# Performance work log

Hardware: AMD Instinct MI355X
Metric: run time of the kernel (lower is better)

Reference implementation:

```python
import jax, jax.numpy as jnp
import numpy as np

C, H, OUT = 64, 128, 64          # in_channels, hidden_dim, out_channels
N, E = 20000, 640000             # nodes, edges
LN_EPS = 1e-5


def layer_norm(x, g, b):
    mu = jnp.mean(x, axis=-1, keepdims=True)
    var = jnp.var(x, axis=-1, keepdims=True)
    return (x - mu) * jax.lax.rsqrt(var + LN_EPS) * g + b


def setup_inputs() -> dict:
    key = jax.random.key(0)
    ks = jax.random.split(key, 12)
    F = 2 * C + 5  # edge MLP input dim = 133

    def w(k, shape, fan_in):
        return jax.random.normal(k, shape, jnp.float32) / np.float32(np.sqrt(fan_in))

    return {
        "x": jax.random.normal(ks[0], (N, C), jnp.float32),
        "pos": jax.random.normal(ks[1], (N, 2), jnp.float32),
        "vel": jax.random.normal(ks[2], (N, 2), jnp.float32),
        # phi_e: Linear(F,H) -> LN -> Softplus -> Linear(H,H) -> Softplus -> Linear(H,H)
        "We1": w(ks[3], (F, H), F), "be1": jnp.zeros((H,), jnp.float32),
        "ge1": jnp.ones((H,), jnp.float32), "bte1": jnp.zeros((H,), jnp.float32),
        "We2": w(ks[4], (H, H), H), "be2": jnp.zeros((H,), jnp.float32),
        "We3": w(ks[5], (H, H), H), "be3": jnp.zeros((H,), jnp.float32),
        # phi_v: Linear(F,H) -> LN -> Softplus -> Linear(H,1)
        "Wv1": w(ks[6], (F, H), F), "bv1": jnp.zeros((H,), jnp.float32),
        "gv1": jnp.ones((H,), jnp.float32), "btv1": jnp.zeros((H,), jnp.float32),
        "Wv2": w(ks[7], (H, 1), H), "bv2": jnp.zeros((1,), jnp.float32),
        # phi_h: Linear(C+H+1,H) -> LN -> Softplus -> Linear(H,OUT)
        "Wh1": w(ks[8], (C + H + 1, H), C + H + 1), "bh1": jnp.zeros((H,), jnp.float32),
        "gh1": jnp.ones((H,), jnp.float32), "bth1": jnp.zeros((H,), jnp.float32),
        "Wh2": w(ks[9], (H, OUT), H), "bh2": jnp.zeros((OUT,), jnp.float32),
        "edge_index": jax.random.randint(ks[10], (2, E), 0, N, dtype=jnp.int64)
        if jax.config.jax_enable_x64 else jax.random.randint(ks[10], (2, E), 0, N, dtype=jnp.int32),
    }


def reference(x, pos, vel,
              We1, be1, ge1, bte1, We2, be2, We3, be3,
              Wv1, bv1, gv1, btv1, Wv2, bv2,
              Wh1, bh1, gh1, bth1, Wh2, bh2,
              edge_index):
    src = edge_index[0]  # j (source / x_j)
    dst = edge_index[1]  # i (target / x_i, aggregation index)

    # per-edge geometric features (gather)
    rel_pos = pos[src] - pos[dst]                                   # [E,2]
    rel_vel = vel[src] - vel[dst]                                   # [E,2]
    dist_sq = jnp.sum(rel_pos ** 2, axis=-1, keepdims=True)         # [E,1]
    dot_vr = jnp.sum(rel_vel * rel_pos, axis=-1, keepdims=True)     # [E,1]
    r2_inv = jnp.minimum(1.0 / (dist_sq + 0.05), 20.0)
    r6_inv = jnp.minimum(r2_inv ** 3, 400.0)
    r12_inv = jnp.minimum(r6_inv ** 2, 160000.0)

    tmp = jnp.concatenate([x[dst], x[src], dist_sq, dot_vr,
                           r2_inv, r6_inv, r12_inv], axis=1)        # [E, 2C+5]

    # phi_e (edge MLP)
    h = jax.nn.softplus(layer_norm(tmp @ We1 + be1, ge1, bte1))
    h = jax.nn.softplus(h @ We2 + be2)
    m_h_e = h @ We3 + be3                                           # [E,H]

    # phi_v (scalar weight on rel_pos -> equivariant vector message)
    v = jax.nn.softplus(layer_norm(tmp @ Wv1 + bv1, gv1, btv1))
    v_w = v @ Wv2 + bv2                                             # [E,1]
    m_v_e = v_w * rel_pos                                           # [E,2]

    # scatter-mean aggregation to target nodes
    n_nodes = x.shape[0]
    ones = jnp.ones((src.shape[0], 1), x.dtype)
    cnt = jax.ops.segment_sum(ones, dst, num_segments=n_nodes)
    denom = jnp.maximum(cnt, 1.0)
    m_h = jax.ops.segment_sum(m_h_e, dst, num_segments=n_nodes) / denom   # [N,H]
    m_v = jax.ops.segment_sum(m_v_e, dst, num_segments=n_nodes) / denom   # [N,2]

    m_v_norm = jnp.sqrt(jnp.sum((m_v + 1e-8) ** 2, axis=-1, keepdims=True))  # [N,1]

    # phi_h (node update MLP); shortcut is Identity since C == OUT
    hin = jnp.concatenate([x, m_h, m_v_norm], axis=-1)              # [N, C+H+1]
    hu = jax.nn.softplus(layer_norm(hin @ Wh1 + bh1, gh1, bth1))
    h_update = hu @ Wh2 + bh2                                       # [N,OUT]
    return x + h_update
```

## Files before the change

### kernel.cpp

```cpp
#include <hip/hip_runtime.h>
#include <stdint.h>

#define NCH    64
#define HID    128
#define OUTC   64
#define NNODE  20000
#define NEDGE  640000
#define FDIM   133
#define TE     32
#define TN     32
#define LN_EPS 1e-5f
#define KP1    160
#define KP2    128
#define KN1    224
#define CAGS   130

typedef __attribute__((ext_vector_type(8))) short bf16x8;
typedef __attribute__((ext_vector_type(4))) float f32x4;

__device__ __forceinline__ unsigned short f2bf(float f) {
    union { float f; unsigned int i; } v; v.f = f;
    unsigned int b = v.i;
    return (unsigned short)((b + 0x7FFFu + ((b >> 16) & 1u)) >> 16);
}
#if defined(__has_builtin)
#if __has_builtin(__builtin_amdgcn_cvt_pk_bf16_f32)
#define HAVE_PK_BF16 1
#endif
#endif
__device__ __forceinline__ unsigned int f2bf_pk(float a, float b) {
#ifdef HAVE_PK_BF16
    auto r = __builtin_amdgcn_cvt_pk_bf16_f32(a, b);
    return __builtin_bit_cast(unsigned int, r);
#else
    return (unsigned int)f2bf(a) | ((unsigned int)f2bf(b) << 16);
#endif
}
__device__ __forceinline__ float bfu2f(unsigned short u) {
    union { unsigned int i; float f; } v; v.i = ((unsigned int)u) << 16; return v.f;
}
__device__ __forceinline__ float sp(float xv) {
    return fmaxf(xv, 0.f) + __logf(1.0f + __expf(-fabsf(xv)));
}
__device__ __forceinline__ void atomAddF(float* p, float v) {
    __hip_atomic_fetch_add(p, v, __ATOMIC_RELAXED, __HIP_MEMORY_SCOPE_AGENT);
}
__device__ __forceinline__ int fragOff(int ks, int mt, int lanepos) {
    return ((ks * 2 + mt) * 64 + lanepos) * 8;
}

#define WT_WE1 0
#define WT_WV1 (128 * KP1)
#define WT_WE2 (2 * 128 * KP1)
#define WT_WE3 (2 * 128 * KP1 + 128 * KP2)
#define WT_WH1 (2 * 128 * KP1 + 2 * 128 * KP2)
#define WT_WH2 (WT_WH1 + 128 * KN1)
#define WT_TOTAL (WT_WH2 + 64 * KP2)

__global__ __launch_bounds__(256)
void eg_prep(const float* __restrict__ We1, const float* __restrict__ Wv1,
             const float* __restrict__ We2, const float* __restrict__ We3,
             const float* __restrict__ Wh1, const float* __restrict__ Wh2,
             short* __restrict__ wt)
{
    int idx = blockIdx.x * 256 + threadIdx.x;
    if (idx >= WT_TOTAL) return;
    if (idx < WT_WV1) {
        int n = idx / KP1, k = idx % KP1;
        wt[idx] = (k < FDIM) ? (short)f2bf(We1[(size_t)k * HID + n]) : (short)0;
    } else if (idx < WT_WE2) {
        int r = idx - WT_WV1; int n = r / KP1, k = r % KP1;
        wt[idx] = (k < FDIM) ? (short)f2bf(Wv1[(size_t)k * HID + n]) : (short)0;
    } else if (idx < WT_WE3) {
        int r = idx - WT_WE2; int n = r / KP2, k = r % KP2;
        wt[idx] = (short)f2bf(We2[(size_t)k * HID + n]);
    } else if (idx < WT_WH1) {
        int r = idx - WT_WE3; int n = r / KP2, k = r % KP2;
        wt[idx] = (short)f2bf(We3[(size_t)k * HID + n]);
    } else if (idx < WT_WH2) {
        int r = idx - WT_WH1; int n = r / KN1, k = r % KN1;
        wt[idx] = (k < 193) ? (short)f2bf(Wh1[(size_t)k * HID + n]) : (short)0;
    } else {
        int r = idx - WT_WH2; int n = r / KP2, k = r % KP2;
        wt[idx] = (short)f2bf(Wh2[(size_t)k * OUTC + n]);
    }
}

__global__ __launch_bounds__(256)
void eg_hist(const int* __restrict__ ei, int* __restrict__ deg)
{
    int i = blockIdx.x * 256 + threadIdx.x;
    if (i < NEDGE)
        __hip_atomic_fetch_add(&deg[ei[NEDGE + i]], 1, __ATOMIC_RELAXED, __HIP_MEMORY_SCOPE_AGENT);
}

__global__ __launch_bounds__(1024)
void eg_scan(const int* __restrict__ deg, int* __restrict__ cur)
{
    __shared__ int part[1024];
    const int tid = threadIdx.x;
    const int chunk = (NNODE + 1023) / 1024;
    const int base = tid * chunk;
    const int lim = min(base + chunk, NNODE);
    int s = 0;
    for (int j = base; j < lim; ++j) s += deg[j];
    part[tid] = s;
    __syncthreads();
    for (int off = 1; off < 1024; off <<= 1) {
        int v = (tid >= off) ? part[tid - off] : 0;
        __syncthreads();
        part[tid] += v;
        __syncthreads();
    }
    int run = (tid > 0) ? part[tid - 1] : 0;
    for (int j = base; j < lim; ++j) { cur[j] = run; run += deg[j]; }
}

__global__ __launch_bounds__(256)
void eg_scatter(const int* __restrict__ ei, int* __restrict__ cur,
                int* __restrict__ perm)
{
    int i = blockIdx.x * 256 + threadIdx.x;
    if (i < NEDGE) {
        int d = ei[NEDGE + i];
        int p = __hip_atomic_fetch_add(&cur[d], 1, __ATOMIC_RELAXED, __HIP_MEMORY_SCOPE_AGENT);
        perm[p] = i;
    }
}

__global__ __launch_bounds__(256, 7)
void eg_edge(const float* __restrict__ x, const float* __restrict__ pos,
             const float* __restrict__ vel,
             const float* __restrict__ be1, const float* __restrict__ ge1,
             const float* __restrict__ bte1, const float* __restrict__ be2,
             const float* __restrict__ be3,
             const float* __restrict__ bv1, const float* __restrict__ gv1,
             const float* __restrict__ btv1,
             const float* __restrict__ Wv2, const float* __restrict__ bv2,
             const short* __restrict__ wt,
             const int* __restrict__ ei, const int* __restrict__ perm,
             float* __restrict__ mh, float* __restrict__ mv)
{
    __shared__ __align__(16) short frag_s[5 * 2 * 64 * 8];
    __shared__ __align__(4) unsigned short cagg_s[TE * CAGS];
    __shared__ float psum_s[512];
    __shared__ float mu_s[64], rs_s[64];
    __shared__ int   dst_s[TE], src_s[TE];
    __shared__ float rel_s[TE * 2], vw_s[TE];

    const int tid  = threadIdx.x;
    const int lane = tid & 63;
    const int wid  = tid >> 6;
    const int lr   = lane & 15;
    const int quad = lane >> 4;
    const int n0w  = wid * 32;
    const int e_base = blockIdx.x * TE;

    const short* We1T = wt + WT_WE1;
    const short* Wv1T = wt + WT_WV1;
    const short* We2T = wt + WT_WE2;
    const short* We3T = wt + WT_WE3;

    float geo[5];
    if (tid < TE) {
        int gi = perm[e_base + tid];
        int eS = ei[gi];
        int eD = ei[NEDGE + gi];
        src_s[tid] = eS; dst_s[tid] = eD;
        float rx = pos[2 * eS]     - pos[2 * eD];
        float ry = pos[2 * eS + 1] - pos[2 * eD + 1];
        float vx = vel[2 * eS]     - vel[2 * eD];
        float vy = vel[2 * eS + 1] - vel[2 * eD + 1];
        float dsq = rx * rx + ry * ry;
        float dvr = vx * rx + vy * ry;
        float r2  = fminf(1.0f / (dsq + 0.05f), 20.0f);
        float r6  = fminf(r2 * r2 * r2, 400.0f);
        float r12 = fminf(r6 * r6, 160000.0f);
        geo[0] = dsq; geo[1] = dvr; geo[2] = r2; geo[3] = r6; geo[4] = r12;
        rel_s[2 * tid] = rx; rel_s[2 * tid + 1] = ry;
    }
    if (tid < 128) {
        int4 z = {0, 0, 0, 0};
        *(int4*)&frag_s[4 * 2 * 64 * 8 + tid * 8] = z;
    }
    __syncthreads();

    if (tid < TE) {
        int off = fragOff(4, tid >> 4, (tid & 15));
        #pragma unroll
        for (int j = 0; j < 5; ++j) frag_s[off + j] = (short)f2bf(geo[j]);
    }
    {
        const int e = tid & 31, slot = tid >> 5;
        const int d = dst_s[e], s = src_s[e];
        #pragma unroll
        for (int h = 0; h < 2; ++h) {
            int o = slot + h * 8;
            int node = h ? s : d;
            int c0 = (o & 7) * 8;
            const float4 a0 = *(const float4*)&x[(size_t)node * NCH + c0];
            const float4 a1 = *(const float4*)&x[(size_t)node * NCH + c0 + 4];
            uint4 pk;
            pk.x = f2bf_pk(a0.x, a0.y); pk.y = f2bf_pk(a0.z, a0.w);
            pk.z = f2bf_pk(a1.x, a1.y); pk.w = f2bf_pk(a1.z, a1.w);
            int ks = o >> 2, kq = o & 3;
            *(uint4*)&frag_s[fragOff(ks, e >> 4, kq * 16 + (e & 15))] = pk;
        }
    }
    __syncthreads();

    const int ncol0 = n0w + lr;
    const int ncol1 = n0w + 16 + lr;

    f32x4 zero4 = {0.f, 0.f, 0.f, 0.f};
    f32x4 accE[2][2], accV[2][2];
    #pragma unroll
    for (int mt = 0; mt < 2; ++mt)
        #pragma unroll
        for (int nt = 0; nt < 2; ++nt) { accE[mt][nt] = zero4; accV[mt][nt] = zero4; }
    for (int ks = 0; ks < 5; ++ks) {
        bf16x8 af0 = *(const bf16x8*)&frag_s[fragOff(ks, 0, lane)];
        bf16x8 af1 = *(const bf16x8*)&frag_s[fragOff(ks, 1, lane)];
        int krow = ks * 32 + quad * 8;
        #pragma unroll
        for (int nt = 0; nt < 2; ++nt) {
            int n = n0w + nt * 16 + lr;
            bf16x8 bwE = *(const bf16x8*)&We1T[n * KP1 + krow];
            bf16x8 bwV = *(const bf16x8*)&Wv1T[n * KP1 + krow];
            accE[0][nt] = __builtin_amdgcn_mfma_f32_16x16x32_bf16(af0, bwE, accE[0][nt], 0, 0, 0);
            accE[1][nt] = __builtin_amdgcn_mfma_f32_16x16x32_bf16(af1, bwE, accE[1][nt], 0, 0, 0);
            accV[0][nt] = __builtin_amdgcn_mfma_f32_16x16x32_bf16(af0, bwV, accV[0][nt], 0, 0, 0);
            accV[1][nt] = __builtin_amdgcn_mfma_f32_16x16x32_bf16(af1, bwV, accV[1][nt], 0, 0, 0);
        }
    }
    {
        float be0 = be1[ncol0], be_1 = be1[ncol1];
        float bv0 = bv1[ncol0], bv_1 = bv1[ncol1];
        #pragma unroll
        for (int mt = 0; mt < 2; ++mt)
            #pragma unroll
            for (int r = 0; r < 4; ++r) {
                accE[mt][0][r] += be0; accE[mt][1][r] += be_1;
                accV[mt][0][r] += bv0; accV[mt][1][r] += bv_1;
            }
    }

    #pragma unroll
    for (int mt = 0; mt < 2; ++mt)
        #pragma unroll
        for (int r = 0; r < 4; ++r) {
            float se = accE[mt][0][r] + accE[mt][1][r];
            float qe = accE[mt][0][r] * accE[mt][0][r] + accE[mt][1][r] * accE[mt][1][r];
            float sv = accV[mt][0][r] + accV[mt][1][r];
            float qv = accV[mt][0][r] * accV[mt][0][r] + accV[mt][1][r] * accV[mt][1][r];
            #pragma unroll
            for (int m = 1; m < 16; m <<= 1) {
                se += __shfl_xor(se, m, 16);
                qe += __shfl_xor(qe, m, 16);
                sv += __shfl_xor(sv, m, 16);
                qv += __shfl_xor(qv, m, 16);
            }
            if (lr == 0) {
                int row = mt * 16 + quad * 4 + r;
                psum_s[      row * 4 + wid] = se;
                psum_s[128 + row * 4 + wid] = qe;
                psum_s[256 + row * 4 + wid] = sv;
                psum_s[384 + row * 4 + wid] = qv;
            }
        }
    __syncthreads();
    if (tid < 64) {
        int p = tid >> 5, row = tid & 31;
        float s = 0.f, q = 0.f;
        #pragma unroll
        for (int w = 0; w < 4; ++w) {
            s += psum_s[p * 256 +       row * 4 + w];
            q += psum_s[p * 256 + 128 + row * 4 + w];
        }
        float mu = s * (1.0f / HID);
        float var = q * (1.0f / HID) - mu * mu;
        mu_s[p * 32 + row] = mu;
        rs_s[p * 32 + row] = rsqrtf(var + LN_EPS);
    }
    __syncthreads();

    {
        float gE0 = ge1[ncol0], gE1 = ge1[ncol1];
        float tE0 = bte1[ncol0], tE1 = bte1[ncol1];
        float gV0 = gv1[ncol0], gV1 = gv1[ncol1];
        float tV0 = btv1[ncol0], tV1 = btv1[ncol1];
        float w20 = Wv2[ncol0], w21 = Wv2[ncol1];
        int ks0 = ncol0 >> 5, kq0 = (ncol0 & 31) >> 3, j0 = ncol0 & 7;
        int ks1 = ncol1 >> 5, kq1 = (ncol1 & 31) >> 3, j1 = ncol1 & 7;
        int fo0 = (ks0 * 128 + kq0 * 16) * 8 + j0;
        int fo1 = (ks1 * 128 + kq1 * 16) * 8 + j1;
        #pragma unroll
        for (int mt = 0; mt < 2; ++mt)
            #pragma unroll
            for (int r = 0; r < 4; ++r) {
                int rlow = quad * 4 + r, row = mt * 16 + rlow;
                float mu = mu_s[row], rsv = rs_s[row];
                float muV = mu_s[32 + row], rsV = rs_s[32 + row];
                float h0 = sp((accE[mt][0][r] - mu) * rsv * gE0 + tE0);
                float h1 = sp((accE[mt][1][r] - mu) * rsv * gE1 + tE1);
                unsigned int ph = f2bf_pk(h0, h1);
                frag_s[fo0 + (mt * 64 + rlow) * 8] = (short)(ph & 0xFFFFu);
                frag_s[fo1 + (mt * 64 + rlow) * 8] = (short)(ph >> 16);
                float v0 = sp((accV[mt][0][r] - muV) * rsV * gV0 + tV0);
                float v1 = sp((accV[mt][1][r] - muV) * rsV * gV1 + tV1);
                float vp = v0 * w20 + v1 * w21;
                #pragma unroll
                for (int m = 1; m < 16; m <<= 1) vp += __shfl_xor(vp, m, 16);
                if (lr == 0) psum_s[row * 4 + wid] = vp;
            }
    }
    __syncthreads();
    if (tid < TE) {
        float s = 0.f;
        #pragma unroll
        for (int w = 0; w < 4; ++w) s += psum_s[tid * 4 + w];
        vw_s[tid] = s + bv2[0];
    }

    {
        f32x4 acc2[2][2];
        #pragma unroll
        for (int mt = 0; mt < 2; ++mt)
            #pragma unroll
            for (int nt = 0; nt < 2; ++nt) acc2[mt][nt] = zero4;
        for (int ks = 0; ks < 4; ++ks) {
            bf16x8 af0 = *(const bf16x8*)&frag_s[fragOff(ks, 0, lane)];
            bf16x8 af1 = *(const bf16x8*)&frag_s[fragOff(ks, 1, lane)];
            int krow = ks * 32 + quad * 8;
            #pragma unroll
            for (int nt = 0; nt < 2; ++nt) {
                int n = n0w + nt * 16 + lr;
                bf16x8 bw = *(const bf16x8*)&We2T[n * KP2 + krow];
                acc2[0][nt] = __builtin_amdgcn_mfma_f32_16x16x32_bf16(af0, bw, acc2[0][nt], 0, 0, 0);
                acc2[1][nt] = __builtin_amdgcn_mfma_f32_16x16x32_bf16(af1, bw, acc2[1][nt], 0, 0, 0);
            }
        }
        __syncthreads();
        #pragma unroll
        for (int nt = 0; nt < 2; ++nt) {
            int kg = n0w + nt * 16 + lr;
            float b2 = be2[kg];
            int ks = kg >> 5, kq = (kg & 31) >> 3, j = kg & 7;
            #pragma unroll
            for (int mt = 0; mt < 2; ++mt) {
                unsigned int u0 = f2bf_pk(sp(acc2[mt][nt][0] + b2), sp(acc2[mt][nt][1] + b2));
                unsigned int u1 = f2bf_pk(sp(acc2[mt][nt][2] + b2), sp(acc2[mt][nt][3] + b2));
                frag_s[fragOff(ks, mt, kq * 16 + quad * 4 + 0) + j] = (short)(u0 & 0xFFFFu);
                frag_s[fragOff(ks, mt, kq * 16 + quad * 4 + 1) + j] = (short)(u0 >> 16);
                frag_s[fragOff(ks, mt, kq * 16 + quad * 4 + 2) + j] = (short)(u1 & 0xFFFFu);
                frag_s[fragOff(ks, mt, kq * 16 + quad * 4 + 3) + j] = (short)(u1 >> 16);
            }
        }
    }
    __syncthreads();

    {
        f32x4 acc3[2][2];
        #pragma unroll
        for (int mt = 0; mt < 2; ++mt)
            #pragma unroll
            for (int nt = 0; nt < 2; ++nt) acc3[mt][nt] = zero4;
        for (int ks = 0; ks < 4; ++ks) {
            bf16x8 af0 = *(const bf16x8*)&frag_s[fragOff(ks, 0, lane)];
            bf16x8 af1 = *(const bf16x8*)&frag_s[fragOff(ks, 1, lane)];
            int krow = ks * 32 + quad * 8;
            #pragma unroll
            for (int nt = 0; nt < 2; ++nt) {
                int n = n0w + nt * 16 + lr;
                bf16x8 bw = *(const bf16x8*)&We3T[n * KP2 + krow];
                acc3[0][nt] = __builtin_amdgcn_mfma_f32_16x16x32_bf16(af0, bw, acc3[0][nt], 0, 0, 0);
                acc3[1][nt] = __builtin_amdgcn_mfma_f32_16x16x32_bf16(af1, bw, acc3[1][nt], 0, 0, 0);
            }
        }
        #pragma unroll
        for (int nt = 0; nt < 2; ++nt) {
            int n = n0w + nt * 16 + lr;
            float b3 = be3[n];
            #pragma unroll
            for (int mt = 0; mt < 2; ++mt) {
                int mb = mt * 16 + quad * 4;
                unsigned int u0 = f2bf_pk(acc3[mt][nt][0] + b3, acc3[mt][nt][1] + b3);
                unsigned int u1 = f2bf_pk(acc3[mt][nt][2] + b3, acc3[mt][nt][3] + b3);
                cagg_s[(mb + 0) * CAGS + n] = (unsigned short)(u0 & 0xFFFFu);
                cagg_s[(mb + 1) * CAGS + n] = (unsigned short)(u0 >> 16);
                cagg_s[(mb + 2) * CAGS + n] = (unsigned short)(u1 & 0xFFFFu);
                cagg_s[(mb + 3) * CAGS + n] = (unsigned short)(u1 >> 16);
            }
        }
    }
    __syncthreads();

    {
        const int c = tid & 127, h = tid >> 7;
        const int m0 = h * 16;
        float run = bfu2f(cagg_s[m0 * CAGS + c]);
        int curd = dst_s[m0];
        #pragma unroll
        for (int m = m0 + 1; m < m0 + 16; ++m) {
            int d = dst_s[m];
            float v = bfu2f(cagg_s[m * CAGS + c]);
            if (d == curd) run += v;
            else { atomAddF(&mh[(size_t)curd * HID + c], run); curd = d; run = v; }
        }
        atomAddF(&mh[(size_t)curd * HID + c], run);
    }
    if (tid < 2) {
        const int c = tid;
        float run = vw_s[0] * rel_s[c];
        int curd = dst_s[0];
        for (int m = 1; m < TE; ++m) {
            int d = dst_s[m];
            float v = vw_s[m] * rel_s[2 * m + c];
            if (d == curd) run += v;
            else { atomAddF(&mv[2 * curd + c], run); curd = d; run = v; }
        }
        atomAddF(&mv[2 * curd + c], run);
    }
}

__global__ __launch_bounds__(256, 7)
void eg_node(const float* __restrict__ x,
             const float* __restrict__ bh1, const float* __restrict__ gh1,
             const float* __restrict__ bth1, const float* __restrict__ bh2,
             const float* __restrict__ mh, const float* __restrict__ mv,
             const int* __restrict__ deg, const short* __restrict__ wt,
             float* __restrict__ out)
{
    __shared__ __align__(16) short frag_s[7 * 2 * 64 * 8];
    __shared__ float psum_s[256];
    __shared__ float mu_s[32], rs_s[32];
    __shared__ float rden_s[TN], norm_s[TN];

    const int tid  = threadIdx.x;
    const int lane = tid & 63;
    const int wid  = tid >> 6;
    const int lr   = lane & 15;
    const int quad = lane >> 4;
    const int n0w  = wid * 32;
    const int n_base = blockIdx.x * TN;

    const short* Wh1T = wt + WT_WH1;
    const short* Wh2T = wt + WT_WH2;

    if (tid < TN) {
        int n = n_base + tid;
        float den = fmaxf((float)deg[n], 1.0f);
        float rd = 1.0f / den;
        float ax = mv[2 * n] * rd + 1e-8f;
        float ay = mv[2 * n + 1] * rd + 1e-8f;
        rden_s[tid] = rd;
        norm_s[tid] = sqrtf(ax * ax + ay * ay);
    }
    if (tid < 128) {
        int4 z = {0, 0, 0, 0};
        *(int4*)&frag_s[6 * 2 * 64 * 8 + tid * 8] = z;
    }
    __syncthreads();

    {
        const int e = tid & 31, slot = tid >> 5;
        const int n = n_base + e;
        {
            int c0 = slot * 8;
            const float4 a0 = *(const float4*)&x[(size_t)n * NCH + c0];
            const float4 a1 = *(const float4*)&x[(size_t)n * NCH + c0 + 4];
            uint4 pk;
            pk.x = f2bf_pk(a0.x, a0.y); pk.y = f2bf_pk(a0.z, a0.w);
            pk.z = f2bf_pk(a1.x, a1.y); pk.w = f2bf_pk(a1.z, a1.w);
            int ks = slot >> 2, kq = slot & 3;
            *(uint4*)&frag_s[fragOff(ks, e >> 4, kq * 16 + (e & 15))] = pk;
        }
        float rd = rden_s[e];
        #pragma unroll
        for (int h = 0; h < 2; ++h) {
            int o = 8 + slot + h * 8;
            int k0 = (o - 8) * 8;
            const float4 a0 = *(const float4*)&mh[(size_t)n * HID + k0];
            const float4 a1 = *(const float4*)&mh[(size_t)n * HID + k0 + 4];
            uint4 pk;
            pk.x = f2bf_pk(a0.x * rd, a0.y * rd); pk.y = f2bf_pk(a0.z * rd, a0.w * rd);
            pk.z = f2bf_pk(a1.x * rd, a1.y * rd); pk.w = f2bf_pk(a1.z * rd, a1.w * rd);
            int ks = o >> 2, kq = o & 3;
            *(uint4*)&frag_s[fragOff(ks, e >> 4, kq * 16 + (e & 15))] = pk;
        }
    }
    if (tid < TN) {
        frag_s[fragOff(6, tid >> 4, (tid & 15))] = (short)f2bf(norm_s[tid]);
    }
    __syncthreads();

    const int ncol0 = n0w + lr;
    const int ncol1 = n0w + 16 + lr;

    f32x4 zero4 = {0.f, 0.f, 0.f, 0.f};
    f32x4 acc1[2][2];
    #pragma unroll
    for (int mt = 0; mt < 2; ++mt)
        #pragma unroll
        for (int nt = 0; nt < 2; ++nt) acc1[mt][nt] = zero4;
    for (int ks = 0; ks < 7; ++ks) {
        bf16x8 af0 = *(const bf16x8*)&frag_s[fragOff(ks, 0, lane)];
        bf16x8 af1 = *(const bf16x8*)&frag_s[fragOff(ks, 1, lane)];
        int krow = ks * 32 + quad * 8;
        #pragma unroll
        for (int nt = 0; nt < 2; ++nt) {
            int n = n0w + nt * 16 + lr;
            bf16x8 bw = *(const bf16x8*)&Wh1T[n * KN1 + krow];
            acc1[0][nt] = __builtin_amdgcn_mfma_f32_16x16x32_bf16(af0, bw, acc1[0][nt], 0, 0, 0);
            acc1[1][nt] = __builtin_amdgcn_mfma_f32_16x16x32_bf16(af1, bw, acc1[1][nt], 0, 0, 0);
        }
    }
    {
        float b0 = bh1[ncol0], b1 = bh1[ncol1];
        #pragma unroll
        for (int mt = 0; mt < 2; ++mt)
            #pragma unroll
            for (int r = 0; r < 4; ++r) { acc1[mt][0][r] += b0; acc1[mt][1][r] += b1; }
    }

    #pragma unroll
    for (int mt = 0; mt < 2; ++mt)
        #pragma unroll
        for (int r = 0; r < 4; ++r) {
            float s = acc1[mt][0][r] + acc1[mt][1][r];
            float q = acc1[mt][0][r] * acc1[mt][0][r] + acc1[mt][1][r] * acc1[mt][1][r];
            #pragma unroll
            for (int m = 1; m < 16; m <<= 1) {
                s += __shfl_xor(s, m, 16);
                q += __shfl_xor(q, m, 16);
            }
            if (lr == 0) {
                int row = mt * 16 + quad * 4 + r;
                psum_s[row * 4 + wid]       = s;
                psum_s[128 + row * 4 + wid] = q;
            }
        }
    __syncthreads();
    if (tid < 32) {
        float s = 0.f, q = 0.f;
        #pragma unroll
        for (int w = 0; w < 4; ++w) {
            s += psum_s[tid * 4 + w];
            q += psum_s[128 + tid * 4 + w];
        }
        float mu = s * (1.0f / HID);
        float var = q * (1.0f / HID) - mu * mu;
        mu_s[tid] = mu;
        rs_s[tid] = rsqrtf(var + LN_EPS);
    }
    __syncthreads();

    {
        float g0 = gh1[ncol0], g1 = gh1[ncol1];
        float t0 = bth1[ncol0], t1 = bth1[ncol1];
        int ks0 = ncol0 >> 5, kq0 = (ncol0 & 31) >> 3, j0 = ncol0 & 7;
        int ks1 = ncol1 >> 5, kq1 = (ncol1 & 31) >> 3, j1 = ncol1 & 7;
        int fo0 = (ks0 * 128 + kq0 * 16) * 8 + j0;
        int fo1 = (ks1 * 128 + kq1 * 16) * 8 + j1;
        #pragma unroll
        for (int mt = 0; mt < 2; ++mt)
            #pragma unroll
            for (int r = 0; r < 4; ++r) {
                int rlow = quad * 4 + r, row = mt * 16 + rlow;
                float mu = mu_s[row], rsv = rs_s[row];
                float h0 = sp((acc1[mt][0][r] - mu) * rsv * g0 + t0);
                float h1 = sp((acc1[mt][1][r] - mu) * rsv * g1 + t1);
                unsigned int ph = f2bf_pk(h0, h1);
                frag_s[fo0 + (mt * 64 + rlow) * 8] = (short)(ph & 0xFFFFu);
                frag_s[fo1 + (mt * 64 + rlow) * 8] = (short)(ph >> 16);
            }
    }
    __syncthreads();

    {
        const int col = wid * 16 + lr;
        f32x4 acc2[2] = { zero4, zero4 };
        for (int ks = 0; ks < 4; ++ks) {
            bf16x8 af0 = *(const bf16x8*)&frag_s[fragOff(ks, 0, lane)];
            bf16x8 af1 = *(const bf16x8*)&frag_s[fragOff(ks, 1, lane)];
            int krow = ks * 32 + quad * 8;
            bf16x8 bw = *(const bf16x8*)&Wh2T[col * KP2 + krow];
            acc2[0] = __builtin_amdgcn_mfma_f32_16x16x32_bf16(af0, bw, acc2[0], 0, 0, 0);
            acc2[1] = __builtin_amdgcn_mfma_f32_16x16x32_bf16(af1, bw, acc2[1], 0, 0, 0);
        }
        float bo = bh2[col];
        #pragma unroll
        for (int mt = 0; mt < 2; ++mt)
            #pragma unroll
            for (int r = 0; r < 4; ++r) {
                int m = mt * 16 + quad * 4 + r;
                size_t idx = (size_t)(n_base + m) * OUTC + col;
                out[idx] = x[(size_t)(n_base + m) * NCH + col] + acc2[mt][r] + bo;
            }
    }
}

extern "C" void kernel_launch(void* const* d_in, const int* in_sizes, int n_in,
                              void* d_out, int out_size, void* d_ws, size_t ws_size,
                              hipStream_t stream)
{
    const float* x    = (const float*)d_in[0];
    const float* pos  = (const float*)d_in[1];
    const float* vel  = (const float*)d_in[2];
    const float* We1  = (const float*)d_in[3];
    const float* be1  = (const float*)d_in[4];
    const float* ge1  = (const float*)d_in[5];
    const float* bte1 = (const float*)d_in[6];
    const float* We2  = (const float*)d_in[7];
    const float* be2  = (const float*)d_in[8];
    const float* We3  = (const float*)d_in[9];
    const float* be3  = (const float*)d_in[10];
    const float* Wv1  = (const float*)d_in[11];
    const float* bv1  = (const float*)d_in[12];
    const float* gv1  = (const float*)d_in[13];
    const float* btv1 = (const float*)d_in[14];
    const float* Wv2  = (const float*)d_in[15];
    const float* bv2  = (const float*)d_in[16];
    const float* Wh1  = (const float*)d_in[17];
    const float* bh1  = (const float*)d_in[18];
    const float* gh1  = (const float*)d_in[19];
    const float* bth1 = (const float*)d_in[20];
    const float* Wh2  = (const float*)d_in[21];
    const float* bh2  = (const float*)d_in[22];
    const int*   ei   = (const int*)d_in[23];

    float* mh   = (float*)d_ws;
    float* mv   = mh + (size_t)NNODE * HID;
    int*   deg  = (int*)(mv + NNODE * 2);
    int*   cur  = deg + NNODE;
    int*   perm = cur + NNODE;
    short* wt   = (short*)(perm + NEDGE);

    size_t zbytes = ((size_t)NNODE * HID + NNODE * 2 + NNODE) * sizeof(float);
    hipMemsetAsync(d_ws, 0, zbytes, stream);

    eg_prep<<<dim3((WT_TOTAL + 255) / 256), dim3(256), 0, stream>>>(
        We1, Wv1, We2, We3, Wh1, Wh2, wt);
    eg_hist<<<dim3(NEDGE / 256), dim3(256), 0, stream>>>(ei, deg);
    eg_scan<<<dim3(1), dim3(1024), 0, stream>>>(deg, cur);
    eg_scatter<<<dim3(NEDGE / 256), dim3(256), 0, stream>>>(ei, cur, perm);

    eg_edge<<<dim3(NEDGE / TE), dim3(256), 0, stream>>>(
        x, pos, vel, be1, ge1, bte1, be2, be3,
        bv1, gv1, btv1, Wv2, bv2, wt, ei, perm, mh, mv);

    eg_node<<<dim3(NNODE / TN), dim3(256), 0, stream>>>(
        x, bh1, gh1, bth1, bh2, mh, mv, deg, wt, (float*)d_out);
}
```

Before: 542.5 us.

## Fuse prep and histogram kernels, pack params, swizzle blocks, unroll MFMA loops

Merges the weight-conversion and degree-histogram kernels into one launch and packs all small bias/LN parameters into one contiguous buffer read through base pointers. Remaps edge-kernel block IDs with an 8-way stride, replaces shfl_xor reductions with ds_swizzle, and fully unrolls the MFMA K-loops with precomputed pointers. The aim is fewer launches, less address arithmetic and cheaper reductions. The block remap changes which edges share an XCD and cache, which can help or hurt atomic locality.

New measurement: 517.7 us. -4.6%, faster.

```diff
diff --git a/kernel.cpp b/kernel.cpp
--- a/kernel.cpp
+++ b/kernel.cpp
@@ -14,6 +14,8 @@
 #define KP2    128
 #define KN1    224
 #define CAGS   130
+#define NEBLK  (NEDGE / TE)
+#define XSTR   (NEBLK / 8)
 
 typedef __attribute__((ext_vector_type(8))) short bf16x8;
 typedef __attribute__((ext_vector_type(4))) float f32x4;
@@ -45,6 +47,12 @@
 __device__ __forceinline__ void atomAddF(float* p, float v) {
     __hip_atomic_fetch_add(p, v, __ATOMIC_RELAXED, __HIP_MEMORY_SCOPE_AGENT);
 }
+template<int PAT> __device__ __forceinline__ float shx(float v) {
+    int i = __builtin_amdgcn_ds_swizzle(__builtin_bit_cast(int, v), PAT);
+    return __builtin_bit_cast(float, i);
+}
+#define RED16(v) { v += shx<0x041F>(v); v += shx<0x081F>(v); v += shx<0x101F>(v); v += shx<0x201F>(v); }
+
 __device__ __forceinline__ int fragOff(int ks, int mt, int lanepos) {
     return ((ks * 2 + mt) * 64 + lanepos) * 8;
 }
@@ -56,42 +64,64 @@
 #define WT_WH1 (2 * 128 * KP1 + 2 * 128 * KP2)
 #define WT_WH2 (WT_WH1 + 128 * KN1)
 #define WT_TOTAL (WT_WH2 + 64 * KP2)
+#define PKP_N  1153
 
 __global__ __launch_bounds__(256)
 void eg_prep(const float* __restrict__ We1, const float* __restrict__ Wv1,
              const float* __restrict__ We2, const float* __restrict__ We3,
              const float* __restrict__ Wh1, const float* __restrict__ Wh2,
-             short* __restrict__ wt)
+             const float* __restrict__ be1, const float* __restrict__ bv1,
+             const float* __restrict__ ge1, const float* __restrict__ bte1,
+             const float* __restrict__ gv1, const float* __restrict__ btv1,
+             const float* __restrict__ Wv2, const float* __restrict__ be2,
+             const float* __restrict__ be3, const float* __restrict__ bv2,
+             const int* __restrict__ ei,
+             short* __restrict__ wt, float* __restrict__ pkp,
+             int* __restrict__ deg)
 {
     int idx = blockIdx.x * 256 + threadIdx.x;
-    if (idx >= WT_TOTAL) return;
-    if (idx < WT_WV1) {
-        int n = idx / KP1, k = idx % KP1;
-        wt[idx] = (k < FDIM) ? (short)f2bf(We1[(size_t)k * HID + n]) : (short)0;
-    } else if (idx < WT_WE2) {
-        int r = idx - WT_WV1; int n = r / KP1, k = r % KP1;
-        wt[idx] = (k < FDIM) ? (short)f2bf(Wv1[(size_t)k * HID + n]) : (short)0;
-    } else if (idx < WT_WE3) {
-        int r = idx - WT_WE2; int n = r / KP2, k = r % KP2;
-        wt[idx] = (short)f2bf(We2[(size_t)k * HID + n]);
-    } else if (idx < WT_WH1) {
-        int r = idx - WT_WE3; int n = r / KP2, k = r % KP2;
-        wt[idx] = (short)f2bf(We3[(size_t)k * HID + n]);
-    } else if (idx < WT_WH2) {
-        int r = idx - WT_WH1; int n = r / KN1, k = r % KN1;
-        wt[idx] = (k < 193) ? (short)f2bf(Wh1[(size_t)k * HID + n]) : (short)0;
-    } else {
-        int r = idx - WT_WH2; int n = r / KP2, k = r % KP2;
-        wt[idx] = (short)f2bf(Wh2[(size_t)k * OUTC + n]);
-    }
-}
-
-__global__ __launch_bounds__(256)
-void eg_hist(const int* __restrict__ ei, int* __restrict__ deg)
-{
-    int i = blockIdx.x * 256 + threadIdx.x;
-    if (i < NEDGE)
-        __hip_atomic_fetch_add(&deg[ei[NEDGE + i]], 1, __ATOMIC_RELAXED, __HIP_MEMORY_SCOPE_AGENT);
+    if (idx < WT_TOTAL) {
+        short v;
+        if (idx < WT_WV1) {
+            int n = idx / KP1, k = idx % KP1;
+            v = (k < FDIM) ? (short)f2bf(We1[(size_t)k * HID + n]) : (short)0;
+        } else if (idx < WT_WE2) {
+            int r = idx - WT_WV1; int n = r / KP1, k = r % KP1;
+            v = (k < FDIM) ? (short)f2bf(Wv1[(size_t)k * HID + n]) : (short)0;
+        } else if (idx < WT_WE3) {
+            int r = idx - WT_WE2; int n = r / KP2, k = r % KP2;
+            v = (short)f2bf(We2[(size_t)k * HID + n]);
+        } else if (idx < WT_WH1) {
+            int r = idx - WT_WE3; int n = r / KP2, k = r % KP2;
+            v = (short)f2bf(We3[(size_t)k * HID + n]);
+        } else if (idx < WT_WH2) {
+            int r = idx - WT_WH1; int n = r / KN1, k = r % KN1;
+            v = (k < 193) ? (short)f2bf(Wh1[(size_t)k * HID + n]) : (short)0;
+        } else {
+            int r = idx - WT_WH2; int n = r / KP2, k = r % KP2;
+            v = (short)f2bf(Wh2[(size_t)k * OUTC + n]);
+        }
+        wt[idx] = v;
+    }
+    if (idx < PKP_N) {
+        float pv;
+        int k = idx >> 7, c = idx & 127;
+        switch (k) {
+            case 0: pv = be1[c]; break;
+            case 1: pv = bv1[c]; break;
+            case 2: pv = ge1[c]; break;
+            case 3: pv = bte1[c]; break;
+            case 4: pv = gv1[c]; break;
+            case 5: pv = btv1[c]; break;
+            case 6: pv = Wv2[c]; break;
+            case 7: pv = be2[c]; break;
+            case 8: pv = be3[c]; break;
+            default: pv = bv2[0]; break;
+        }
+        pkp[idx] = pv;
+    }
+    if (idx < NEDGE)
+        __hip_atomic_fetch_add(&deg[ei[NEDGE + idx]], 1, __ATOMIC_RELAXED, __HIP_MEMORY_SCOPE_AGENT);
 }
 
 __global__ __launch_bounds__(1024)
@@ -131,12 +161,7 @@
 __global__ __launch_bounds__(256, 7)
 void eg_edge(const float* __restrict__ x, const float* __restrict__ pos,
              const float* __restrict__ vel,
-             const float* __restrict__ be1, const float* __restrict__ ge1,
-             const float* __restrict__ bte1, const float* __restrict__ be2,
-             const float* __restrict__ be3,
-             const float* __restrict__ bv1, const float* __restrict__ gv1,
-             const float* __restrict__ btv1,
-             const float* __restrict__ Wv2, const float* __restrict__ bv2,
+             const float* __restrict__ pkp,
              const short* __restrict__ wt,
              const int* __restrict__ ei, const int* __restrict__ perm,
              float* __restrict__ mh, float* __restrict__ mv)
@@ -154,7 +179,8 @@
     const int lr   = lane & 15;
     const int quad = lane >> 4;
     const int n0w  = wid * 32;
-    const int e_base = blockIdx.x * TE;
+    const int bid  = (blockIdx.x & 7) * XSTR + (blockIdx.x >> 3);
+    const int e_base = bid * TE;
 
     const short* We1T = wt + WT_WE1;
     const short* Wv1T = wt + WT_WV1;
@@ -211,6 +237,8 @@
 
     const int ncol0 = n0w + lr;
     const int ncol1 = n0w + 16 + lr;
+    const float* p0 = pkp + ncol0;
+    const float* p1 = pkp + ncol1;
 
     f32x4 zero4 = {0.f, 0.f, 0.f, 0.f};
     f32x4 accE[2][2], accV[2][2];
@@ -218,24 +246,33 @@
     for (int mt = 0; mt < 2; ++mt)
         #pragma unroll
         for (int nt = 0; nt < 2; ++nt) { accE[mt][nt] = zero4; accV[mt][nt] = zero4; }
-    for (int ks = 0; ks < 5; ++ks) {
-        bf16x8 af0 = *(const bf16x8*)&frag_s[fragOff(ks, 0, lane)];
-        bf16x8 af1 = *(const bf16x8*)&frag_s[fragOff(ks, 1, lane)];
-        int krow = ks * 32 + quad * 8;
-        #pragma unroll
-        for (int nt = 0; nt < 2; ++nt) {
-            int n = n0w + nt * 16 + lr;
-            bf16x8 bwE = *(const bf16x8*)&We1T[n * KP1 + krow];
-            bf16x8 bwV = *(const bf16x8*)&Wv1T[n * KP1 + krow];
-            accE[0][nt] = __builtin_amdgcn_mfma_f32_16x16x32_bf16(af0, bwE, accE[0][nt], 0, 0, 0);
-            accE[1][nt] = __builtin_amdgcn_mfma_f32_16x16x32_bf16(af1, bwE, accE[1][nt], 0, 0, 0);
-            accV[0][nt] = __builtin_amdgcn_mfma_f32_16x16x32_bf16(af0, bwV, accV[0][nt], 0, 0, 0);
-            accV[1][nt] = __builtin_amdgcn_mfma_f32_16x16x32_bf16(af1, bwV, accV[1][nt], 0, 0, 0);
-        }
-    }
-    {
-        float be0 = be1[ncol0], be_1 = be1[ncol1];
-        float bv0 = bv1[ncol0], bv_1 = bv1[ncol1];
+    {
+        const short* pa = &frag_s[lane * 8];
+        const short* pwE0 = We1T + ncol0 * KP1 + quad * 8;
+        const short* pwE1 = We1T + ncol1 * KP1 + quad * 8;
+        const short* pwV0 = Wv1T + ncol0 * KP1 + quad * 8;
+        const short* pwV1 = Wv1T + ncol1 * KP1 + quad * 8;
+        #pragma unroll
+        for (int ks = 0; ks < 5; ++ks) {
+            bf16x8 af0 = *(const bf16x8*)&pa[ks * 1024];
+            bf16x8 af1 = *(const bf16x8*)&pa[ks * 1024 + 512];
+            bf16x8 bwE0 = *(const bf16x8*)&pwE0[ks * 32];
+            bf16x8 bwE1 = *(const bf16x8*)&pwE1[ks * 32];
+            bf16x8 bwV0 = *(const bf16x8*)&pwV0[ks * 32];
+            bf16x8 bwV1 = *(const bf16x8*)&pwV1[ks * 32];
+            accE[0][0] = __builtin_amdgcn_mfma_f32_16x16x32_bf16(af0, bwE0, accE[0][0], 0, 0, 0);
+            accE[1][0] = __builtin_amdgcn_mfma_f32_16x16x32_bf16(af1, bwE0, accE[1][0], 0, 0, 0);
+            accE[0][1] = __builtin_amdgcn_mfma_f32_16x16x32_bf16(af0, bwE1, accE[0][1], 0, 0, 0);
+            accE[1][1] = __builtin_amdgcn_mfma_f32_16x16x32_bf16(af1, bwE1, accE[1][1], 0, 0, 0);
+            accV[0][0] = __builtin_amdgcn_mfma_f32_16x16x32_bf16(af0, bwV0, accV[0][0], 0, 0, 0);
+            accV[1][0] = __builtin_amdgcn_mfma_f32_16x16x32_bf16(af1, bwV0, accV[1][0], 0, 0, 0);
+            accV[0][1] = __builtin_amdgcn_mfma_f32_16x16x32_bf16(af0, bwV1, accV[0][1], 0, 0, 0);
+            accV[1][1] = __builtin_amdgcn_mfma_f32_16x16x32_bf16(af1, bwV1, accV[1][1], 0, 0, 0);
+        }
+    }
+    {
+        float be0 = p0[0], be_1 = p1[0];
+        float bv0 = p0[128], bv_1 = p1[128];
         #pragma unroll
         for (int mt = 0; mt < 2; ++mt)
             #pragma unroll
@@ -253,13 +290,7 @@
             float qe = accE[mt][0][r] * accE[mt][0][r] + accE[mt][1][r] * accE[mt][1][r];
             float sv = accV[mt][0][r] + accV[mt][1][r];
             float qv = accV[mt][0][r] * accV[mt][0][r] + accV[mt][1][r] * accV[mt][1][r];
-            #pragma unroll
-            for (int m = 1; m < 16; m <<= 1) {
-                se += __shfl_xor(se, m, 16);
-                qe += __shfl_xor(qe, m, 16);
-                sv += __shfl_xor(sv, m, 16);
-                qv += __shfl_xor(qv, m, 16);
-            }
+            RED16(se); RED16(qe); RED16(sv); RED16(qv);
             if (lr == 0) {
                 int row = mt * 16 + quad * 4 + r;
                 psum_s[      row * 4 + wid] = se;
@@ -285,15 +316,15 @@
     __syncthreads();
 
     {
-        float gE0 = ge1[ncol0], gE1 = ge1[ncol1];
-        float tE0 = bte1[ncol0], tE1 = bte1[ncol1];
-        float gV0 = gv1[ncol0], gV1 = gv1[ncol1];
-        float tV0 = btv1[ncol0], tV1 = btv1[ncol1];
-        float w20 = Wv2[ncol0], w21 = Wv2[ncol1];
+        float gE0 = p0[256], gE1 = p1[256];
+        float tE0 = p0[384], tE1 = p1[384];
+        float gV0 = p0[512], gV1 = p1[512];
+        float tV0 = p0[640], tV1 = p1[640];
+        float w20 = p0[768], w21 = p1[768];
         int ks0 = ncol0 >> 5, kq0 = (ncol0 & 31) >> 3, j0 = ncol0 & 7;
         int ks1 = ncol1 >> 5, kq1 = (ncol1 & 31) >> 3, j1 = ncol1 & 7;
-        int fo0 = (ks0 * 128 + kq0 * 16) * 8 + j0;
-        int fo1 = (ks1 * 128 + kq1 * 16) * 8 + j1;
+        short* bp0 = &frag_s[(ks0 * 128 + kq0 * 16 + quad * 4) * 8 + j0];
+        short* bp1 = &frag_s[(ks1 * 128 + kq1 * 16 + quad * 4) * 8 + j1];
         #pragma unroll
         for (int mt = 0; mt < 2; ++mt)
             #pragma unroll
@@ -304,13 +335,12 @@
                 float h0 = sp((accE[mt][0][r] - mu) * rsv * gE0 + tE0);
                 float h1 = sp((accE[mt][1][r] - mu) * rsv * gE1 + tE1);
                 unsigned int ph = f2bf_pk(h0, h1);
-                frag_s[fo0 + (mt * 64 + rlow) * 8] = (short)(ph & 0xFFFFu);
-                frag_s[fo1 + (mt * 64 + rlow) * 8] = (short)(ph >> 16);
+                bp0[mt * 512 + r * 8] = (short)(ph & 0xFFFFu);
+                bp1[mt * 512 + r * 8] = (short)(ph >> 16);
                 float v0 = sp((accV[mt][0][r] - muV) * rsV * gV0 + tV0);
                 float v1 = sp((accV[mt][1][r] - muV) * rsV * gV1 + tV1);
                 float vp = v0 * w20 + v1 * w21;
-                #pragma unroll
-                for (int m = 1; m < 16; m <<= 1) vp += __shfl_xor(vp, m, 16);
+                RED16(vp);
                 if (lr == 0) psum_s[row * 4 + wid] = vp;
             }
     }
@@ -319,7 +349,7 @@
         float s = 0.f;
         #pragma unroll
         for (int w = 0; w < 4; ++w) s += psum_s[tid * 4 + w];
-        vw_s[tid] = s + bv2[0];
+        vw_s[tid] = s + pkp[1152];
     }
 
     {
@@ -328,34 +358,35 @@
         for (int mt = 0; mt < 2; ++mt)
             #pragma unroll
             for (int nt = 0; nt < 2; ++nt) acc2[mt][nt] = zero4;
-        for (int ks = 0; ks < 4; ++ks) {
-            bf16x8 af0 = *(const bf16x8*)&frag_s[fragOff(ks, 0, lane)];
-            bf16x8 af1 = *(const bf16x8*)&frag_s[fragOff(ks, 1, lane)];
-            int krow = ks * 32 + quad * 8;
-            #pragma unroll
-            for (int nt = 0; nt < 2; ++nt) {
-                int n = n0w + nt * 16 + lr;
-                bf16x8 bw = *(const bf16x8*)&We2T[n * KP2 + krow];
-                acc2[0][nt] = __builtin_amdgcn_mfma_f32_16x16x32_bf16(af0, bw, acc2[0][nt], 0, 0, 0);
-                acc2[1][nt] = __builtin_amdgcn_mfma_f32_16x16x32_bf16(af1, bw, acc2[1][nt], 0, 0, 0);
+        {
+            const short* pa = &frag_s[lane * 8];
+            const short* pw0 = We2T + ncol0 * KP2 + quad * 8;
+            const short* pw1 = We2T + ncol1 * KP2 + quad * 8;
+            #pragma unroll
+            for (int ks = 0; ks < 4; ++ks) {
+                bf16x8 af0 = *(const bf16x8*)&pa[ks * 1024];
+                bf16x8 af1 = *(const bf16x8*)&pa[ks * 1024 + 512];
+                bf16x8 bw0 = *(const bf16x8*)&pw0[ks * 32];
+                bf16x8 bw1 = *(const bf16x8*)&pw1[ks * 32];
+                acc2[0][0] = __builtin_amdgcn_mfma_f32_16x16x32_bf16(af0, bw0, acc2[0][0], 0, 0, 0);
+                acc2[1][0] = __builtin_amdgcn_mfma_f32_16x16x32_bf16(af1, bw0, acc2[1][0], 0, 0, 0);
+                acc2[0][1] = __builtin_amdgcn_mfma_f32_16x16x32_bf16(af0, bw1, acc2[0][1], 0, 0, 0);
+                acc2[1][1] = __builtin_amdgcn_mfma_f32_16x16x32_bf16(af1, bw1, acc2[1][1], 0, 0, 0);
             }
         }
         __syncthreads();
-        #pragma unroll
-        for (int nt = 0; nt < 2; ++nt) {
-            int kg = n0w + nt * 16 + lr;
-            float b2 = be2[kg];
-            int ks = kg >> 5, kq = (kg & 31) >> 3, j = kg & 7;
-            #pragma unroll
-            for (int mt = 0; mt < 2; ++mt) {
-                unsigned int u0 = f2bf_pk(sp(acc2[mt][nt][0] + b2), sp(acc2[mt][nt][1] + b2));
-                unsigned int u1 = f2bf_pk(sp(acc2[mt][nt][2] + b2), sp(acc2[mt][nt][3] + b2));
-                frag_s[fragOff(ks, mt, kq * 16 + quad * 4 + 0) + j] = (short)(u0 & 0xFFFFu);
-                frag_s[fragOff(ks, mt, kq * 16 + quad * 4 + 1) + j] = (short)(u0 >> 16);
-                frag_s[fragOff(ks, mt, kq * 16 + quad * 4 + 2) + j] = (short)(u1 & 0xFFFFu);
-                frag_s[fragOff(ks, mt, kq * 16 + quad * 4 + 3) + j] = (short)(u1 >> 16);
-            }
-        }
+        float b2a = p0[896], b2b = p1[896];
+        int ksA = ncol0 >> 5, kqA = (ncol0 & 31) >> 3, jA = ncol0 & 7;
+        int ksB = ncol1 >> 5, kqB = (ncol1 & 31) >> 3, jB = ncol1 & 7;
+        short* bpA = &frag_s[(ksA * 128 + kqA * 16 + quad * 4) * 8 + jA];
+        short* bpB = &frag_s[(ksB * 128 + kqB * 16 + quad * 4) * 8 + jB];
+        #pragma unroll
+        for (int mt = 0; mt < 2; ++mt)
+            #pragma unroll
+            for (int r = 0; r < 4; ++r) {
+                bpA[mt * 512 + r * 8] = (short)f2bf(sp(acc2[mt][0][r] + b2a));
+                bpB[mt * 512 + r * 8] = (short)f2bf(sp(acc2[mt][1][r] + b2b));
+            }
     }
     __syncthreads();
 
@@ -365,45 +396,45 @@
         for (int mt = 0; mt < 2; ++mt)
             #pragma unroll
             for (int nt = 0; nt < 2; ++nt) acc3[mt][nt] = zero4;
-        for (int ks = 0; ks < 4; ++ks) {
-            bf16x8 af0 = *(const bf16x8*)&frag_s[fragOff(ks, 0, lane)];
-            bf16x8 af1 = *(const bf16x8*)&frag_s[fragOff(ks, 1, lane)];
-            int krow = ks * 32 + quad * 8;
-            #pragma unroll
-            for (int nt = 0; nt < 2; ++nt) {
-                int n = n0w + nt * 16 + lr;
-                bf16x8 bw = *(const bf16x8*)&We3T[n * KP2 + krow];
-                acc3[0][nt] = __builtin_amdgcn_mfma_f32_16x16x32_bf16(af0, bw, acc3[0][nt], 0, 0, 0);
-                acc3[1][nt] = __builtin_amdgcn_mfma_f32_16x16x32_bf16(af1, bw, acc3[1][nt], 0, 0, 0);
-            }
-        }
-        #pragma unroll
-        for (int nt = 0; nt < 2; ++nt) {
-            int n = n0w + nt * 16 + lr;
-            float b3 = be3[n];
-            #pragma unroll
-            for (int mt = 0; mt < 2; ++mt) {
-                int mb = mt * 16 + quad * 4;
-                unsigned int u0 = f2bf_pk(acc3[mt][nt][0] + b3, acc3[mt][nt][1] + b3);
-                unsigned int u1 = f2bf_pk(acc3[mt][nt][2] + b3, acc3[mt][nt][3] + b3);
-                cagg_s[(mb + 0) * CAGS + n] = (unsigned short)(u0 & 0xFFFFu);
-                cagg_s[(mb + 1) * CAGS + n] = (unsigned short)(u0 >> 16);
-                cagg_s[(mb + 2) * CAGS + n] = (unsigned short)(u1 & 0xFFFFu);
-                cagg_s[(mb + 3) * CAGS + n] = (unsigned short)(u1 >> 16);
-            }
-        }
+        {
+            const short* pa = &frag_s[lane * 8];
+            const short* pw0 = We3T + ncol0 * KP2 + quad * 8;
+            const short* pw1 = We3T + ncol1 * KP2 + quad * 8;
+            #pragma unroll
+            for (int ks = 0; ks < 4; ++ks) {
+                bf16x8 af0 = *(const bf16x8*)&pa[ks * 1024];
+                bf16x8 af1 = *(const bf16x8*)&pa[ks * 1024 + 512];
+                bf16x8 bw0 = *(const bf16x8*)&pw0[ks * 32];
+                bf16x8 bw1 = *(const bf16x8*)&pw1[ks * 32];
+                acc3[0][0] = __builtin_amdgcn_mfma_f32_16x16x32_bf16(af0, bw0, acc3[0][0], 0, 0, 0);
+                acc3[1][0] = __builtin_amdgcn_mfma_f32_16x16x32_bf16(af1, bw0, acc3[1][0], 0, 0, 0);
+                acc3[0][1] = __builtin_amdgcn_mfma_f32_16x16x32_bf16(af0, bw1, acc3[0][1], 0, 0, 0);
+                acc3[1][1] = __builtin_amdgcn_mfma_f32_16x16x32_bf16(af1, bw1, acc3[1][1], 0, 0, 0);
+            }
+        }
+        float b3a = p0[1024], b3b = p1[1024];
+        unsigned short* bpA = &cagg_s[(quad * 4) * CAGS + ncol0];
+        unsigned short* bpB = &cagg_s[(quad * 4) * CAGS + ncol1];
+        #pragma unroll
+        for (int mt = 0; mt < 2; ++mt)
+            #pragma unroll
+            for (int r = 0; r < 4; ++r) {
+                bpA[(mt * 16 + r) * CAGS] = f2bf(acc3[mt][0][r] + b3a);
+                bpB[(mt * 16 + r) * CAGS] = f2bf(acc3[mt][1][r] + b3b);
+            }
     }
     __syncthreads();
 
     {
         const int c = tid & 127, h = tid >> 7;
+        const unsigned short* cp = &cagg_s[(h * 16) * CAGS + c];
         const int m0 = h * 16;
-        float run = bfu2f(cagg_s[m0 * CAGS + c]);
+        float run = bfu2f(cp[0]);
         int curd = dst_s[m0];
         #pragma unroll
-        for (int m = m0 + 1; m < m0 + 16; ++m) {
-            int d = dst_s[m];
-            float v = bfu2f(cagg_s[m * CAGS + c]);
+        for (int m = 1; m < 16; ++m) {
+            int d = dst_s[m0 + m];
+            float v = bfu2f(cp[m * CAGS]);
             if (d == curd) run += v;
             else { atomAddF(&mh[(size_t)curd * HID + c], run); curd = d; run = v; }
         }
@@ -503,16 +534,20 @@
     for (int mt = 0; mt < 2; ++mt)
         #pragma unroll
         for (int nt = 0; nt < 2; ++nt) acc1[mt][nt] = zero4;
-    for (int ks = 0; ks < 7; ++ks) {
-        bf16x8 af0 = *(const bf16x8*)&frag_s[fragOff(ks, 0, lane)];
-        bf16x8 af1 = *(const bf16x8*)&frag_s[fragOff(ks, 1, lane)];
-        int krow = ks * 32 + quad * 8;
-        #pragma unroll
-        for (int nt = 0; nt < 2; ++nt) {
-            int n = n0w + nt * 16 + lr;
-            bf16x8 bw = *(const bf16x8*)&Wh1T[n * KN1 + krow];
-            acc1[0][nt] = __builtin_amdgcn_mfma_f32_16x16x32_bf16(af0, bw, acc1[0][nt], 0, 0, 0);
-            acc1[1][nt] = __builtin_amdgcn_mfma_f32_16x16x32_bf16(af1, bw, acc1[1][nt], 0, 0, 0);
+    {
+        const short* pa = &frag_s[lane * 8];
+        const short* pw0 = Wh1T + ncol0 * KN1 + quad * 8;
+        const short* pw1 = Wh1T + ncol1 * KN1 + quad * 8;
+        #pragma unroll
+        for (int ks = 0; ks < 7; ++ks) {
+            bf16x8 af0 = *(const bf16x8*)&pa[ks * 1024];
+            bf16x8 af1 = *(const bf16x8*)&pa[ks * 1024 + 512];
+            bf16x8 bw0 = *(const bf16x8*)&pw0[ks * 32];
+            bf16x8 bw1 = *(const bf16x8*)&pw1[ks * 32];
+            acc1[0][0] = __builtin_amdgcn_mfma_f32_16x16x32_bf16(af0, bw0, acc1[0][0], 0, 0, 0);
+            acc1[1][0] = __builtin_amdgcn_mfma_f32_16x16x32_bf16(af1, bw0, acc1[1][0], 0, 0, 0);
+            acc1[0][1] = __builtin_amdgcn_mfma_f32_16x16x32_bf16(af0, bw1, acc1[0][1], 0, 0, 0);
+            acc1[1][1] = __builtin_amdgcn_mfma_f32_16x16x32_bf16(af1, bw1, acc1[1][1], 0, 0, 0);
         }
     }
     {
@@ -529,11 +564,7 @@
         for (int r = 0; r < 4; ++r) {
             float s = acc1[mt][0][r] + acc1[mt][1][r];
             float q = acc1[mt][0][r] * acc1[mt][0][r] + acc1[mt][1][r] * acc1[mt][1][r];
-            #pragma unroll
-            for (int m = 1; m < 16; m <<= 1) {
-                s += __shfl_xor(s, m, 16);
-                q += __shfl_xor(q, m, 16);
-            }
+            RED16(s); RED16(q);
             if (lr == 0) {
                 int row = mt * 16 + quad * 4 + r;
                 psum_s[row * 4 + wid]       = s;
@@ -560,19 +591,19 @@
         float t0 = bth1[ncol0], t1 = bth1[ncol1];
         int ks0 = ncol0 >> 5, kq0 = (ncol0 & 31) >> 3, j0 = ncol0 & 7;
         int ks1 = ncol1 >> 5, kq1 = (ncol1 & 31) >> 3, j1 = ncol1 & 7;
-        int fo0 = (ks0 * 128 + kq0 * 16) * 8 + j0;
-        int fo1 = (ks1 * 128 + kq1 * 16) * 8 + j1;
+        short* bp0 = &frag_s[(ks0 * 128 + kq0 * 16 + quad * 4) * 8 + j0];
+        short* bp1 = &frag_s[(ks1 * 128 + kq1 * 16 + quad * 4) * 8 + j1];
         #pragma unroll
         for (int mt = 0; mt < 2; ++mt)
             #pragma unroll
             for (int r = 0; r < 4; ++r) {
-                int rlow = quad * 4 + r, row = mt * 16 + rlow;
+                int row = mt * 16 + quad * 4 + r;
                 float mu = mu_s[row], rsv = rs_s[row];
                 float h0 = sp((acc1[mt][0][r] - mu) * rsv * g0 + t0);
                 float h1 = sp((acc1[mt][1][r] - mu) * rsv * g1 + t1);
                 unsigned int ph = f2bf_pk(h0, h1);
-                frag_s[fo0 + (mt * 64 + rlow) * 8] = (short)(ph & 0xFFFFu);
-                frag_s[fo1 + (mt * 64 + rlow) * 8] = (short)(ph >> 16);
+                bp0[mt * 512 + r * 8] = (short)(ph & 0xFFFFu);
+                bp1[mt * 512 + r * 8] = (short)(ph >> 16);
             }
     }
     __syncthreads();
@@ -580,11 +611,13 @@
     {
         const int col = wid * 16 + lr;
         f32x4 acc2[2] = { zero4, zero4 };
+        const short* pa = &frag_s[lane * 8];
+        const short* pw = Wh2T + col * KP2 + quad * 8;
+        #pragma unroll
         for (int ks = 0; ks < 4; ++ks) {
-            bf16x8 af0 = *(const bf16x8*)&frag_s[fragOff(ks, 0, lane)];
-            bf16x8 af1 = *(const bf16x8*)&frag_s[fragOff(ks, 1, lane)];
-            int krow = ks * 32 + quad * 8;
-            bf16x8 bw = *(const bf16x8*)&Wh2T[col * KP2 + krow];
+            bf16x8 af0 = *(const bf16x8*)&pa[ks * 1024];
+            bf16x8 af1 = *(const bf16x8*)&pa[ks * 1024 + 512];
+            bf16x8 bw = *(const bf16x8*)&pw[ks * 32];
             acc2[0] = __builtin_amdgcn_mfma_f32_16x16x32_bf16(af0, bw, acc2[0], 0, 0, 0);
             acc2[1] = __builtin_amdgcn_mfma_f32_16x16x32_bf16(af1, bw, acc2[1], 0, 0, 0);
         }
@@ -634,20 +667,21 @@
     int*   deg  = (int*)(mv + NNODE * 2);
     int*   cur  = deg + NNODE;
     int*   perm = cur + NNODE;
-    short* wt   = (short*)(perm + NEDGE);
+    float* pkp  = (float*)(perm + NEDGE);
+    short* wt   = (short*)(pkp + 1280);
 
     size_t zbytes = ((size_t)NNODE * HID + NNODE * 2 + NNODE) * sizeof(float);
     hipMemsetAsync(d_ws, 0, zbytes, stream);
 
-    eg_prep<<<dim3((WT_TOTAL + 255) / 256), dim3(256), 0, stream>>>(
-        We1, Wv1, We2, We3, Wh1, Wh2, wt);
-    eg_hist<<<dim3(NEDGE / 256), dim3(256), 0, stream>>>(ei, deg);
+    eg_prep<<<dim3(NEDGE / 256), dim3(256), 0, stream>>>(
+        We1, Wv1, We2, We3, Wh1, Wh2,
+        be1, bv1, ge1, bte1, gv1, btv1, Wv2, be2, be3, bv2,
+        ei, wt, pkp, deg);
     eg_scan<<<dim3(1), dim3(1024), 0, stream>>>(deg, cur);
     eg_scatter<<<dim3(NEDGE / 256), dim3(256), 0, stream>>>(ei, cur, perm);
 
-    eg_edge<<<dim3(NEDGE / TE), dim3(256), 0, stream>>>(
-        x, pos, vel, be1, ge1, bte1, be2, be3,
-        bv1, gv1, btv1, Wv2, bv2, wt, ei, perm, mh, mv);
+    eg_edge<<<dim3(NEBLK), dim3(256), 0, stream>>>(
+        x, pos, vel, pkp, wt, ei, perm, mh, mv);
 
     eg_node<<<dim3(NNODE / TN), dim3(256), 0, stream>>>(
         x, bh1, gh1, bth1, bh2, mh, mv, deg, wt, (float*)d_out);
```
